# Kernel optimization log

Hardware: AMD Instinct MI355X
Metric: run time of the kernel (lower is better)

Reference implementation:

```python
import math
import jax, jax.numpy as jnp
import numpy as np

N_TOKENS = 2048
HIDDEN = 2880
HEAD_DIM = 64
N_HEADS = 64
N_KV = 8
Q_MULT = N_HEADS // N_KV  # 8
SLIDING_WINDOW = 128      # layer_idx=0 -> even -> window active
RMS_EPS = 1e-5
SM_SCALE = 1.0 / math.sqrt(HEAD_DIM)
ROPE_THETA = 150000.0
INIT_CTX = 4096
SCALING_FACTOR = 32.0
NTK_ALPHA = 1.0
NTK_BETA = 32.0
QKV_DIM = HEAD_DIM * (N_HEADS + 2 * N_KV)  # 5120


def _rope_cos_sin(n_tokens):
    # YaRN/NTK-scaled inverse frequencies (scaling_factor > 1 branch)
    freq = ROPE_THETA ** (jnp.arange(0, HEAD_DIM, 2, dtype=jnp.float32) / HEAD_DIM)
    concentration = 0.1 * math.log(SCALING_FACTOR) + 1.0
    d_half = HEAD_DIM / 2
    low = d_half * math.log(INIT_CTX / (NTK_BETA * 2 * math.pi)) / math.log(ROPE_THETA)
    high = d_half * math.log(INIT_CTX / (NTK_ALPHA * 2 * math.pi)) / math.log(ROPE_THETA)
    interpolation = 1.0 / (SCALING_FACTOR * freq)
    extrapolation = 1.0 / freq
    ramp = (jnp.arange(d_half, dtype=jnp.float32) - low) / (high - low)
    mask = 1.0 - jnp.clip(ramp, 0.0, 1.0)
    inv_freq = interpolation * (1.0 - mask) + extrapolation * mask
    pos = jnp.arange(n_tokens, dtype=jnp.float32)
    freqs = pos[:, None] * inv_freq[None, :]        # [n, d/2]
    return jnp.cos(freqs) * concentration, jnp.sin(freqs) * concentration


def _apply_rotary(x, cos, sin):
    # x: [n, h, d]; cos/sin: [n, d/2]
    c = cos[:, None, :]
    s = sin[:, None, :]
    x1, x2 = jnp.split(x, 2, axis=-1)
    return jnp.concatenate([x1 * c - x2 * s, x2 * c + x1 * s], axis=-1)


def setup_inputs() -> dict:
    key = jax.random.key(0)
    ks = jax.random.split(key, 4)
    x = jax.random.normal(ks[0], (N_TOKENS, HIDDEN), dtype=jnp.float32)
    norm_scale = jnp.ones((HIDDEN,), dtype=jnp.float32)
    sinks = jax.random.normal(ks[1], (N_HEADS,), dtype=jnp.float32)
    w_qkv = jax.random.normal(ks[2], (QKV_DIM, HIDDEN), dtype=jnp.float32) * 0.02
    b_qkv = jnp.zeros((QKV_DIM,), dtype=jnp.float32)
    w_out = jax.random.normal(ks[3], (HIDDEN, N_HEADS * HEAD_DIM), dtype=jnp.float32) * 0.02
    b_out = jnp.zeros((HIDDEN,), dtype=jnp.float32)
    return {"x": x, "norm_scale": norm_scale, "sinks": sinks,
            "w_qkv": w_qkv, "b_qkv": b_qkv, "w_out": w_out, "b_out": b_out}


def reference(x, norm_scale, sinks, w_qkv, b_qkv, w_out, b_out):
    n = x.shape[0]
    # RMSNorm (fp32 math as in original)
    t = x.astype(jnp.float32)
    t = t * jax.lax.rsqrt(jnp.mean(t * t, axis=-1, keepdims=True) + RMS_EPS)
    t = (t * norm_scale).astype(x.dtype)
    # QKV projection (torch Linear: y = x @ W^T + b)
    qkv = t @ w_qkv.T + b_qkv
    q = qkv[:, : N_HEADS * HEAD_DIM].reshape(n, N_KV, Q_MULT, HEAD_DIM)
    k = qkv[:, N_HEADS * HEAD_DIM:(N_HEADS + N_KV) * HEAD_DIM].reshape(n, N_KV, HEAD_DIM)
    v = qkv[:, (N_HEADS + N_KV) * HEAD_DIM:].reshape(n, N_KV, HEAD_DIM)
    # RoPE
    cos, sin = _rope_cos_sin(n)
    q = _apply_rotary(q.reshape(n, N_HEADS, HEAD_DIM), cos, sin).reshape(n, N_KV, Q_MULT, HEAD_DIM)
    k = _apply_rotary(k, cos, sin)
    # GQA attention scores: [kv_heads, q_mult, q, k]
    qk = jnp.einsum('qhmd,khd->hmqk', q, k) * SM_SCALE
    # causal + sliding-window mask: allow j <= i and j > i - SLIDING_WINDOW
    i = jnp.arange(n)[:, None]
    j = jnp.arange(n)[None, :]
    allowed = (j <= i) & (j > i - SLIDING_WINDOW)
    neg_inf = jnp.asarray(-jnp.inf, dtype=qk.dtype)
    qk = jnp.where(allowed[None, None, :, :], qk, neg_inf)
    # append learned sink logit per head, softmax, then drop sink column
    sink_logits = jnp.broadcast_to(
        sinks.reshape(N_KV, Q_MULT, 1, 1), (N_KV, Q_MULT, n, 1)).astype(qk.dtype)
    logits = jnp.concatenate([qk, sink_logits], axis=-1)
    weights = jax.nn.softmax(logits, axis=-1)[..., :-1]
    attn = jnp.einsum('hmqk,khd->qhmd', weights, v).reshape(n, N_HEADS * HEAD_DIM)
    return x + attn @ w_out.T + b_out
```

## Files before the change

kernel.cpp:

```cpp
#include <hip/hip_runtime.h>
#include <hip/hip_bf16.h>
#include <math.h>

typedef __attribute__((ext_vector_type(8))) short short8;
typedef __attribute__((ext_vector_type(4))) float f32x4;

#define NTOK 2048
#define HID  2880
#define QKVD 5120
#define KOFF 4096
#define VOFF 4608
#define ATTD 4096

__device__ __forceinline__ unsigned short f2bf(float f) {
  union { float f; unsigned int u; } v; v.f = f;
  unsigned int u = v.u;
  unsigned int r = (u + 0x7FFFu + ((u >> 16) & 1u)) >> 16;
  return (unsigned short)r;
}
__device__ __forceinline__ float bf2f(unsigned short h) {
  union { unsigned int u; float f; } v; v.u = ((unsigned int)h) << 16; return v.f;
}
__device__ __forceinline__ void gload_lds16(const unsigned short* g, unsigned short* l) {
  __builtin_amdgcn_global_load_lds(
      (const __attribute__((address_space(1))) unsigned int*)g,
      (__attribute__((address_space(3))) unsigned int*)l, 16, 0, 0);
}
#define MFMA16(a, b, c) __builtin_amdgcn_mfma_f32_16x16x32_bf16((a), (b), (c), 0, 0, 0)

__global__ void rope_table_kernel(float* __restrict__ ctab, float* __restrict__ stab) {
  int idx = blockIdx.x * 256 + threadIdx.x;
  if (idx >= NTOK * 32) return;
  int pos = idx >> 5, i = idx & 31;
  const double theta = 150000.0;
  const double two_pi = 6.283185307179586476925286766559;
  double freq = pow(theta, (double)i / 32.0);
  double interp = 1.0 / (32.0 * freq);
  double extrap = 1.0 / freq;
  double low  = 32.0 * log(4096.0 / (32.0 * two_pi)) / log(theta);
  double high = 32.0 * log(4096.0 / (1.0  * two_pi)) / log(theta);
  double ramp = ((double)i - low) / (high - low);
  ramp = ramp < 0.0 ? 0.0 : (ramp > 1.0 ? 1.0 : ramp);
  double maskv = 1.0 - ramp;
  double inv = interp * (1.0 - maskv) + extrap * maskv;
  double ang = (double)pos * inv;
  double conc = 0.1 * log(32.0) + 1.0;
  ctab[idx] = (float)(cos(ang) * conc);
  stab[idx] = (float)(sin(ang) * conc);
}

__global__ __launch_bounds__(256) void rmsnorm_kernel(
    const float* __restrict__ x, const float* __restrict__ scale,
    unsigned short* __restrict__ t) {
  int row = blockIdx.x;
  const float4* xr = (const float4*)(x + (size_t)row * HID);
  const float4* sc = (const float4*)scale;
  float ss = 0.f;
  for (int c = threadIdx.x; c < HID / 4; c += 256) {
    float4 v = xr[c];
    ss += v.x * v.x + v.y * v.y + v.z * v.z + v.w * v.w;
  }
  #pragma unroll
  for (int m = 1; m < 64; m <<= 1) ss += __shfl_xor(ss, m);
  __shared__ float red[4];
  if ((threadIdx.x & 63) == 0) red[threadIdx.x >> 6] = ss;
  __syncthreads();
  float tot = red[0] + red[1] + red[2] + red[3];
  float rs = rsqrtf(tot / (float)HID + 1e-5f);
  for (int c = threadIdx.x; c < HID / 4; c += 256) {
    float4 v = xr[c];
    float4 s4 = sc[c];
    ushort4 o;
    o.x = f2bf(v.x * rs * s4.x); o.y = f2bf(v.y * rs * s4.y);
    o.z = f2bf(v.z * rs * s4.z); o.w = f2bf(v.w * rs * s4.w);
    *(ushort4*)&t[(size_t)row * HID + c * 4] = o;
  }
}

__global__ __launch_bounds__(256) void cvt_both_kernel(
    const float* __restrict__ w1, const float* __restrict__ w2,
    unsigned short* __restrict__ o1, unsigned short* __restrict__ o2,
    long n1_4, long total4) {
  long idx = (long)blockIdx.x * 256 + threadIdx.x;
  if (idx >= total4) return;
  const float* src; unsigned short* dst; long base;
  if (idx < n1_4) { src = w1; dst = o1; base = idx * 4; }
  else            { src = w2; dst = o2; base = (idx - n1_4) * 4; }
  float4 v = *(const float4*)&src[base];
  ushort4 o;
  o.x = f2bf(v.x); o.y = f2bf(v.y); o.z = f2bf(v.z); o.w = f2bf(v.w);
  *(ushort4*)&dst[base] = o;
}

template<int BN, bool RESID>
__global__ __launch_bounds__(256, 2) void gemm_kernel(
    const unsigned short* __restrict__ A, const unsigned short* __restrict__ B,
    const float* __restrict__ bias, const float* __restrict__ resid,
    void* __restrict__ Cout, int K, int NC) {
  constexpr int NF = BN / 32;
  __shared__ unsigned short sA[2][8192];
  __shared__ unsigned short sB[2][BN * 64];

  const int tid = threadIdx.x;
  const int q8 = gridDim.x >> 3;
  const int sw = ((int)blockIdx.x & 7) * q8 + ((int)blockIdx.x >> 3);
  const int m0 = (sw & 15) * 128;
  const int n0 = (sw >> 4) * BN;

  const int lane = tid & 63, wid = tid >> 6;
  const int fr = lane & 15, fq = lane >> 4;
  const int wr = wid >> 1, wc = wid & 1;
  const int swz = (fr & 7) << 4;
  const int r_st = tid >> 3;
  const int c8_st = ((tid & 7) ^ ((tid >> 3) & 7)) * 8;
  const int wlds = wid << 9;

  const unsigned short* Ag = A + (size_t)(m0 + r_st) * K + c8_st;
  const unsigned short* Bg = B + (size_t)(n0 + r_st) * K + c8_st;

  f32x4 acc[4][NF] = {};
  const int NT = K >> 6;

  auto LDA_ = [&](int bs, int mf, int ks) -> short8 {
    int row = wr * 64 + mf * 16 + fr;
    int cb = (ks * 64 + fq * 16) ^ swz;
    return *(const short8*)((const char*)&sA[bs][0] + row * 128 + cb);
  };
  auto LDB_ = [&](int bs, int nf, int ks) -> short8 {
    int row = wc * (NF * 16) + nf * 16 + fr;
    int cb = (ks * 64 + fq * 16) ^ swz;
    return *(const short8*)((const char*)&sB[bs][0] + row * 128 + cb);
  };
  auto issue_tile = [&](int tt, int b) {
    const unsigned short* Agt = Ag + (size_t)tt * 64;
    const unsigned short* Bgt = Bg + (size_t)tt * 64;
    #pragma unroll
    for (int s = 0; s < 4; ++s)
      gload_lds16(Agt + (size_t)(s * 32) * K, &sA[b][s * 2048 + wlds]);
    #pragma unroll
    for (int s = 0; s < NF; ++s)
      gload_lds16(Bgt + (size_t)(s * 32) * K, &sB[b][s * 2048 + wlds]);
  };

  issue_tile(0, 0);

  for (int t = 0; t < NT; ++t) {
    const int cu = t & 1;
    asm volatile("s_waitcnt vmcnt(0)" ::: "memory");
    __builtin_amdgcn_s_barrier();
    __builtin_amdgcn_sched_barrier(0);
    if (t + 1 < NT) issue_tile(t + 1, cu ^ 1);
    short8 afr0[4], bfr0[NF], afr1[4], bfr1[NF];
    #pragma unroll
    for (int mf = 0; mf < 4; ++mf) afr0[mf] = LDA_(cu, mf, 0);
    #pragma unroll
    for (int nf = 0; nf < NF; ++nf) bfr0[nf] = LDB_(cu, nf, 0);
    #pragma unroll
    for (int mf = 0; mf < 4; ++mf) afr1[mf] = LDA_(cu, mf, 1);
    #pragma unroll
    for (int nf = 0; nf < NF; ++nf) bfr1[nf] = LDB_(cu, nf, 1);
    __builtin_amdgcn_s_setprio(1);
    #pragma unroll
    for (int mf = 0; mf < 4; ++mf)
      #pragma unroll
      for (int nf = 0; nf < NF; ++nf)
        acc[mf][nf] = MFMA16(afr0[mf], bfr0[nf], acc[mf][nf]);
    #pragma unroll
    for (int mf = 0; mf < 4; ++mf)
      #pragma unroll
      for (int nf = 0; nf < NF; ++nf)
        acc[mf][nf] = MFMA16(afr1[mf], bfr1[nf], acc[mf][nf]);
    __builtin_amdgcn_s_setprio(0);
  }

  if (!RESID) {
    unsigned short* C = (unsigned short*)Cout;
    #pragma unroll
    for (int mf = 0; mf < 4; ++mf)
      #pragma unroll
      for (int nf = 0; nf < NF; ++nf)
        #pragma unroll
        for (int r = 0; r < 4; ++r) {
          int row = m0 + wr * 64 + mf * 16 + fq * 4 + r;
          int col = n0 + wc * (NF * 16) + nf * 16 + fr;
          C[(size_t)row * NC + col] = f2bf(acc[mf][nf][r] + bias[col]);
        }
  } else {
    float* C = (float*)Cout;
    #pragma unroll
    for (int mf = 0; mf < 4; ++mf)
      #pragma unroll
      for (int nf = 0; nf < NF; ++nf)
        #pragma unroll
        for (int r = 0; r < 4; ++r) {
          int row = m0 + wr * 64 + mf * 16 + fq * 4 + r;
          int col = n0 + wc * (NF * 16) + nf * 16 + fr;
          C[(size_t)row * NC + col] = acc[mf][nf][r] + bias[col] + resid[(size_t)row * NC + col];
        }
  }
}

__global__ __launch_bounds__(256) void attn_kernel(
    const unsigned short* __restrict__ qkv, const float* __restrict__ sinks,
    const float* __restrict__ ctab, const float* __restrict__ stab,
    unsigned short* __restrict__ attn) {
  const int tile = blockIdx.x;
  const int gh = blockIdx.y;
  const int h = gh >> 3;
  const int q0 = tile * 64;
  const int kbase = q0 - 127;

  __shared__ unsigned short Qsh[64][72];
  __shared__ unsigned short Ksh[192][72];
  __shared__ unsigned short Vt[64][200];
  __shared__ float rowpart[4][64];
  __shared__ float invsum[64];
  unsigned short (*Wsh)[200] = (unsigned short (*)[200])Ksh;

  const int tid = threadIdx.x;

  {
    int r = tid >> 2, cp = tid & 3;
    int i = q0 + r;
    const unsigned short* qp = &qkv[(size_t)i * QKVD + gh * 64 + cp * 8];
    short8 xa = *(const short8*)qp;
    short8 xb = *(const short8*)(qp + 32);
    short8 oa, ob;
    #pragma unroll
    for (int e = 0; e < 8; ++e) {
      float c = ctab[i * 32 + cp * 8 + e], s = stab[i * 32 + cp * 8 + e];
      float x1 = bf2f((unsigned short)xa[e]), x2 = bf2f((unsigned short)xb[e]);
      oa[e] = (short)f2bf(x1 * c - x2 * s);
      ob[e] = (short)f2bf(x2 * c + x1 * s);
    }
    *(short8*)&Qsh[r][cp * 8] = oa;
    *(short8*)&Qsh[r][cp * 8 + 32] = ob;
  }
  #pragma unroll
  for (int it = 0; it < 3; ++it) {
    int lin = tid + it * 256;
    int r = lin >> 2, cp = lin & 3;
    int j = kbase + r;
    short8 oa = {}, ob = {};
    if (j >= 0 && j < NTOK) {
      const unsigned short* kp = &qkv[(size_t)j * QKVD + KOFF + h * 64 + cp * 8];
      short8 xa = *(const short8*)kp;
      short8 xb = *(const short8*)(kp + 32);
      #pragma unroll
      for (int e = 0; e < 8; ++e) {
        float c = ctab[j * 32 + cp * 8 + e], s = stab[j * 32 + cp * 8 + e];
        float x1 = bf2f((unsigned short)xa[e]), x2 = bf2f((unsigned short)xb[e]);
        oa[e] = (short)f2bf(x1 * c - x2 * s);
        ob[e] = (short)f2bf(x2 * c + x1 * s);
      }
    }
    *(short8*)&Ksh[r][cp * 8] = oa;
    *(short8*)&Ksh[r][cp * 8 + 32] = ob;
  }
  #pragma unroll
  for (int c = 0; c < 6; ++c) {
    int lin = tid + c * 256;
    int r = lin >> 3, ch = (lin & 7) * 8;
    int j = kbase + r;
    uint4 v = make_uint4(0u, 0u, 0u, 0u);
    if (j >= 0 && j < NTOK) v = *(const uint4*)&qkv[(size_t)j * QKVD + VOFF + h * 64 + ch];
    const unsigned short* vs = (const unsigned short*)&v;
    #pragma unroll
    for (int i2 = 0; i2 < 8; ++i2) Vt[ch + i2][r] = vs[i2];
  }
  __syncthreads();

  const int lane = tid & 63;
  const int wid = tid >> 6;
  const int fr = lane & 15;
  const int fq = lane >> 4;
  const int fc = fq * 8;
  const int wk0 = wid * 48;

  f32x4 sc[4][3] = {};
  #pragma unroll
  for (int k0 = 0; k0 < 64; k0 += 32) {
    short8 qa[4], kb[3];
    #pragma unroll
    for (int mi = 0; mi < 4; ++mi) qa[mi] = *(const short8*)&Qsh[mi * 16 + fr][k0 + fc];
    #pragma unroll
    for (int ni = 0; ni < 3; ++ni) kb[ni] = *(const short8*)&Ksh[wk0 + ni * 16 + fr][k0 + fc];
    #pragma unroll
    for (int mi = 0; mi < 4; ++mi)
      #pragma unroll
      for (int ni = 0; ni < 3; ++ni)
        sc[mi][ni] = MFMA16(qa[mi], kb[ni], sc[mi][ni]);
  }

  float rsum[4][4];
  #pragma unroll
  for (int mi = 0; mi < 4; ++mi)
    #pragma unroll
    for (int r = 0; r < 4; ++r) {
      int i = q0 + mi * 16 + fq * 4 + r;
      float rs = 0.f;
      #pragma unroll
      for (int ni = 0; ni < 3; ++ni) {
        int kk = wk0 + ni * 16 + fr;
        int j = kbase + kk;
        bool valid = (j >= 0) && (j <= i) && (j > i - 128);
        float pw = valid ? __expf(sc[mi][ni][r] * 0.125f) : 0.f;
        sc[mi][ni][r] = pw;
        rs += pw;
      }
      rs += __shfl_xor(rs, 1);
      rs += __shfl_xor(rs, 2);
      rs += __shfl_xor(rs, 4);
      rs += __shfl_xor(rs, 8);
      rsum[mi][r] = rs;
    }

  __syncthreads();

  #pragma unroll
  for (int mi = 0; mi < 4; ++mi)
    #pragma unroll
    for (int r = 0; r < 4; ++r) {
      int row = mi * 16 + fq * 4 + r;
      #pragma unroll
      for (int ni = 0; ni < 3; ++ni)
        Wsh[row][wk0 + ni * 16 + fr] = f2bf(sc[mi][ni][r]);
      if (fr == 0) rowpart[wid][row] = rsum[mi][r];
    }
  __syncthreads();

  if (tid < 64) {
    float tot = rowpart[0][tid] + rowpart[1][tid] + rowpart[2][tid] + rowpart[3][tid];
    invsum[tid] = 1.f / (tot + __expf(sinks[gh]));
  }

  f32x4 pv[4] = {};
  #pragma unroll
  for (int k0 = 0; k0 < 192; k0 += 32) {
    short8 pa[4];
    #pragma unroll
    for (int mi = 0; mi < 4; ++mi) pa[mi] = *(const short8*)&Wsh[mi * 16 + fr][k0 + fc];
    short8 vb = *(const short8*)&Vt[wid * 16 + fr][k0 + fc];
    #pragma unroll
    for (int mi = 0; mi < 4; ++mi)
      pv[mi] = MFMA16(pa[mi], vb, pv[mi]);
  }
  __syncthreads();

  #pragma unroll
  for (int mi = 0; mi < 4; ++mi)
    #pragma unroll
    for (int r = 0; r < 4; ++r) {
      int row = mi * 16 + fq * 4 + r;
      float inv = invsum[row];
      int col = wid * 16 + fr;
      attn[(size_t)(q0 + row) * ATTD + gh * 64 + col] = f2bf(pv[mi][r] * inv);
    }
}

extern "C" void kernel_launch(void* const* d_in, const int* in_sizes, int n_in,
                              void* d_out, int out_size, void* d_ws, size_t ws_size,
                              hipStream_t stream) {
  const float* x          = (const float*)d_in[0];
  const float* norm_scale = (const float*)d_in[1];
  const float* sinks      = (const float*)d_in[2];
  const float* w_qkv      = (const float*)d_in[3];
  const float* b_qkv      = (const float*)d_in[4];
  const float* w_out      = (const float*)d_in[5];
  const float* b_out      = (const float*)d_in[6];
  float* out = (float*)d_out;

  char* ws = (char*)d_ws;
  unsigned short* qkv_bf = (unsigned short*)(ws);
  unsigned short* t_bf   = (unsigned short*)(ws + 20971520);
  unsigned short* attn_b = (unsigned short*)(ws + 20971520);
  unsigned short* w1bf   = (unsigned short*)(ws + 20971520 + 16777216);
  unsigned short* w2bf   = w1bf;
  w2bf = (unsigned short*)(ws + 20971520 + 16777216 + 29491200);
  float* ctab = (float*)(ws + 20971520 + 16777216 + 29491200 + 23592960);
  float* stab = ctab + NTOK * 32;

  rope_table_kernel<<<dim3(256), dim3(256), 0, stream>>>(ctab, stab);
  rmsnorm_kernel<<<dim3(NTOK), dim3(256), 0, stream>>>(x, norm_scale, t_bf);
  cvt_both_kernel<<<dim3(25920), dim3(256), 0, stream>>>(
      w_qkv, w_out, w1bf, w2bf, 3686400L, 6635520L);
  gemm_kernel<160, false><<<dim3(512), dim3(256), 0, stream>>>(
      t_bf, w1bf, b_qkv, nullptr, (void*)qkv_bf, HID, QKVD);
  attn_kernel<<<dim3(32, 64), dim3(256), 0, stream>>>(qkv_bf, sinks, ctab, stab, attn_b);
  gemm_kernel<96, true><<<dim3(480), dim3(256), 0, stream>>>(
      attn_b, w2bf, b_out, x, (void*)out, ATTD, HID);
}
```

Baseline: 209.0 us.

## Merge prep kernels and overlap w_out conversion with QKV GEMM blocks

Folds the rope table, rmsnorm, and w_qkv bf16 conversion into a single prep kernel so there are fewer launches. The w_out conversion moves into extra blocks appended to the QKV GEMM grid, letting that memory-bound work run alongside the GEMM tiles. The risk is that these conversion blocks compete with GEMM blocks for CUs. The GEMM tile swizzle now uses an explicit count of GEMM blocks instead of the grid size.

```diff
diff --git a/kernel.cpp b/kernel.cpp
--- a/kernel.cpp
+++ b/kernel.cpp
@@ -28,81 +28,92 @@
 }
 #define MFMA16(a, b, c) __builtin_amdgcn_mfma_f32_16x16x32_bf16((a), (b), (c), 0, 0, 0)
 
-__global__ void rope_table_kernel(float* __restrict__ ctab, float* __restrict__ stab) {
-  int idx = blockIdx.x * 256 + threadIdx.x;
-  if (idx >= NTOK * 32) return;
-  int pos = idx >> 5, i = idx & 31;
-  const double theta = 150000.0;
-  const double two_pi = 6.283185307179586476925286766559;
-  double freq = pow(theta, (double)i / 32.0);
-  double interp = 1.0 / (32.0 * freq);
-  double extrap = 1.0 / freq;
-  double low  = 32.0 * log(4096.0 / (32.0 * two_pi)) / log(theta);
-  double high = 32.0 * log(4096.0 / (1.0  * two_pi)) / log(theta);
-  double ramp = ((double)i - low) / (high - low);
-  ramp = ramp < 0.0 ? 0.0 : (ramp > 1.0 ? 1.0 : ramp);
-  double maskv = 1.0 - ramp;
-  double inv = interp * (1.0 - maskv) + extrap * maskv;
-  double ang = (double)pos * inv;
-  double conc = 0.1 * log(32.0) + 1.0;
-  ctab[idx] = (float)(cos(ang) * conc);
-  stab[idx] = (float)(sin(ang) * conc);
-}
-
-__global__ __launch_bounds__(256) void rmsnorm_kernel(
+__global__ __launch_bounds__(256) void prep_kernel(
     const float* __restrict__ x, const float* __restrict__ scale,
-    unsigned short* __restrict__ t) {
-  int row = blockIdx.x;
-  const float4* xr = (const float4*)(x + (size_t)row * HID);
-  const float4* sc = (const float4*)scale;
-  float ss = 0.f;
-  for (int c = threadIdx.x; c < HID / 4; c += 256) {
-    float4 v = xr[c];
-    ss += v.x * v.x + v.y * v.y + v.z * v.z + v.w * v.w;
-  }
-  #pragma unroll
-  for (int m = 1; m < 64; m <<= 1) ss += __shfl_xor(ss, m);
+    unsigned short* __restrict__ t,
+    const float* __restrict__ w1, unsigned short* __restrict__ w1bf,
+    float* __restrict__ ctab, float* __restrict__ stab) {
   __shared__ float red[4];
-  if ((threadIdx.x & 63) == 0) red[threadIdx.x >> 6] = ss;
-  __syncthreads();
-  float tot = red[0] + red[1] + red[2] + red[3];
-  float rs = rsqrtf(tot / (float)HID + 1e-5f);
-  for (int c = threadIdx.x; c < HID / 4; c += 256) {
-    float4 v = xr[c];
-    float4 s4 = sc[c];
-    ushort4 o;
-    o.x = f2bf(v.x * rs * s4.x); o.y = f2bf(v.y * rs * s4.y);
-    o.z = f2bf(v.z * rs * s4.z); o.w = f2bf(v.w * rs * s4.w);
-    *(ushort4*)&t[(size_t)row * HID + c * 4] = o;
-  }
-}
-
-__global__ __launch_bounds__(256) void cvt_both_kernel(
-    const float* __restrict__ w1, const float* __restrict__ w2,
-    unsigned short* __restrict__ o1, unsigned short* __restrict__ o2,
-    long n1_4, long total4) {
-  long idx = (long)blockIdx.x * 256 + threadIdx.x;
-  if (idx >= total4) return;
-  const float* src; unsigned short* dst; long base;
-  if (idx < n1_4) { src = w1; dst = o1; base = idx * 4; }
-  else            { src = w2; dst = o2; base = (idx - n1_4) * 4; }
-  float4 v = *(const float4*)&src[base];
-  ushort4 o;
-  o.x = f2bf(v.x); o.y = f2bf(v.y); o.z = f2bf(v.z); o.w = f2bf(v.w);
-  *(ushort4*)&dst[base] = o;
+  const int bid = blockIdx.x;
+  const int tid = threadIdx.x;
+  if (bid < 2048) {
+    const float4* xr = (const float4*)(x + (size_t)bid * HID);
+    const float4* sc = (const float4*)scale;
+    float ss = 0.f;
+    for (int c = tid; c < HID / 4; c += 256) {
+      float4 v = xr[c];
+      ss += v.x * v.x + v.y * v.y + v.z * v.z + v.w * v.w;
+    }
+    #pragma unroll
+    for (int m = 1; m < 64; m <<= 1) ss += __shfl_xor(ss, m);
+    if ((tid & 63) == 0) red[tid >> 6] = ss;
+    __syncthreads();
+    float tot = red[0] + red[1] + red[2] + red[3];
+    float rs = rsqrtf(tot / (float)HID + 1e-5f);
+    for (int c = tid; c < HID / 4; c += 256) {
+      float4 v = xr[c];
+      float4 s4 = sc[c];
+      ushort4 o;
+      o.x = f2bf(v.x * rs * s4.x); o.y = f2bf(v.y * rs * s4.y);
+      o.z = f2bf(v.z * rs * s4.z); o.w = f2bf(v.w * rs * s4.w);
+      *(ushort4*)&t[(size_t)bid * HID + c * 4] = o;
+    }
+  } else if (bid < 5648) {
+    long base0 = (long)(bid - 2048) * 1024;
+    #pragma unroll
+    for (int k2 = 0; k2 < 4; ++k2) {
+      long base = (base0 + k2 * 256 + tid) * 4;
+      float4 v = *(const float4*)&w1[base];
+      ushort4 o;
+      o.x = f2bf(v.x); o.y = f2bf(v.y); o.z = f2bf(v.z); o.w = f2bf(v.w);
+      *(ushort4*)&w1bf[base] = o;
+    }
+  } else {
+    int idx = (bid - 5648) * 256 + tid;
+    int pos = idx >> 5, i = idx & 31;
+    const double theta = 150000.0;
+    const double two_pi = 6.283185307179586476925286766559;
+    double freq = pow(theta, (double)i / 32.0);
+    double interp = 1.0 / (32.0 * freq);
+    double extrap = 1.0 / freq;
+    double low  = 32.0 * log(4096.0 / (32.0 * two_pi)) / log(theta);
+    double high = 32.0 * log(4096.0 / (1.0  * two_pi)) / log(theta);
+    double ramp = ((double)i - low) / (high - low);
+    ramp = ramp < 0.0 ? 0.0 : (ramp > 1.0 ? 1.0 : ramp);
+    double maskv = 1.0 - ramp;
+    double inv = interp * (1.0 - maskv) + extrap * maskv;
+    double ang = (double)pos * inv;
+    double conc = 0.1 * log(32.0) + 1.0;
+    ctab[idx] = (float)(cos(ang) * conc);
+    stab[idx] = (float)(sin(ang) * conc);
+  }
 }
 
 template<int BN, bool RESID>
 __global__ __launch_bounds__(256, 2) void gemm_kernel(
     const unsigned short* __restrict__ A, const unsigned short* __restrict__ B,
     const float* __restrict__ bias, const float* __restrict__ resid,
-    void* __restrict__ Cout, int K, int NC) {
+    void* __restrict__ Cout, int K, int NC,
+    const float* __restrict__ cvt_src, unsigned short* __restrict__ cvt_dst,
+    int ngemm) {
   constexpr int NF = BN / 32;
   __shared__ unsigned short sA[2][8192];
   __shared__ unsigned short sB[2][BN * 64];
 
   const int tid = threadIdx.x;
-  const int q8 = gridDim.x >> 3;
+  if ((int)blockIdx.x >= ngemm) {
+    long base0 = (long)((int)blockIdx.x - ngemm) * 1024;
+    #pragma unroll
+    for (int k2 = 0; k2 < 4; ++k2) {
+      long base = (base0 + k2 * 256 + tid) * 4;
+      float4 v = *(const float4*)&cvt_src[base];
+      ushort4 o;
+      o.x = f2bf(v.x); o.y = f2bf(v.y); o.z = f2bf(v.z); o.w = f2bf(v.w);
+      *(ushort4*)&cvt_dst[base] = o;
+    }
+    return;
+  }
+  const int q8 = ngemm >> 3;
   const int sw = ((int)blockIdx.x & 7) * q8 + ((int)blockIdx.x >> 3);
   const int m0 = (sw & 15) * 128;
   const int n0 = (sw >> 4) * BN;
@@ -375,18 +386,17 @@
   unsigned short* t_bf   = (unsigned short*)(ws + 20971520);
   unsigned short* attn_b = (unsigned short*)(ws + 20971520);
   unsigned short* w1bf   = (unsigned short*)(ws + 20971520 + 16777216);
-  unsigned short* w2bf   = w1bf;
-  w2bf = (unsigned short*)(ws + 20971520 + 16777216 + 29491200);
+  unsigned short* w2bf   = (unsigned short*)(ws + 20971520 + 16777216 + 29491200);
   float* ctab = (float*)(ws + 20971520 + 16777216 + 29491200 + 23592960);
   float* stab = ctab + NTOK * 32;
 
-  rope_table_kernel<<<dim3(256), dim3(256), 0, stream>>>(ctab, stab);
-  rmsnorm_kernel<<<dim3(NTOK), dim3(256), 0, stream>>>(x, norm_scale, t_bf);
-  cvt_both_kernel<<<dim3(25920), dim3(256), 0, stream>>>(
-      w_qkv, w_out, w1bf, w2bf, 3686400L, 6635520L);
-  gemm_kernel<160, false><<<dim3(512), dim3(256), 0, stream>>>(
-      t_bf, w1bf, b_qkv, nullptr, (void*)qkv_bf, HID, QKVD);
+  prep_kernel<<<dim3(5904), dim3(256), 0, stream>>>(
+      x, norm_scale, t_bf, w_qkv, w1bf, ctab, stab);
+  gemm_kernel<160, false><<<dim3(3392), dim3(256), 0, stream>>>(
+      t_bf, w1bf, b_qkv, nullptr, (void*)qkv_bf, HID, QKVD,
+      w_out, w2bf, 512);
   attn_kernel<<<dim3(32, 64), dim3(256), 0, stream>>>(qkv_bf, sinks, ctab, stab, attn_b);
   gemm_kernel<96, true><<<dim3(480), dim3(256), 0, stream>>>(
-      attn_b, w2bf, b_out, x, (void*)out, ATTD, HID);
-}
+      attn_b, w2bf, b_out, x, (void*)out, ATTD, HID,
+      nullptr, nullptr, 480);
+}
```

After: 197.1 us. 5.7% less time.
